# Optimization experiments

Hardware: AMD Instinct MI355X
Metric: run time of the kernel (lower is better)

The kernel has to match this reference:

```python
import jax, jax.numpy as jnp
import numpy as np
from jax import lax

M, T, D, E, NTAGS = 512, 512, 128, 512, 74
GH = D // 2   # GRU hidden per direction (64)
LH = E // 2   # LSTM hidden per direction (256)


def _gru_dir(x, Wih, Whh, bih, bhh):
    # x: [T, Din] -> [T, H]; PyTorch gate order r, z, n
    h = Whh.shape[1]
    gi = x @ Wih.T + bih  # [T, 3H] precomputed input projections
    def step(hprev, gi_t):
        gh = hprev @ Whh.T + bhh
        r = jax.nn.sigmoid(gi_t[:h] + gh[:h])
        z = jax.nn.sigmoid(gi_t[h:2 * h] + gh[h:2 * h])
        n = jnp.tanh(gi_t[2 * h:] + r * gh[2 * h:])
        hnew = (1.0 - z) * n + z * hprev
        return hnew, hnew
    _, hs = lax.scan(step, jnp.zeros((h,), x.dtype), gi)
    return hs


def _bigru(x, Wf, Uf, bf, cf, Wb, Ub, bb, cb):
    hf = _gru_dir(x, Wf, Uf, bf, cf)
    hb = _gru_dir(x[::-1], Wb, Ub, bb, cb)[::-1]
    return jnp.concatenate([hf, hb], axis=-1)


def _lstm_dir(x, Wih, Whh, bih, bhh):
    # PyTorch gate order i, f, g, o
    h = Whh.shape[1]
    gi = x @ Wih.T + bih  # [T, 4H]
    def step(carry, gi_t):
        hprev, cprev = carry
        g = gi_t + hprev @ Whh.T + bhh
        i = jax.nn.sigmoid(g[:h])
        f = jax.nn.sigmoid(g[h:2 * h])
        gg = jnp.tanh(g[2 * h:3 * h])
        o = jax.nn.sigmoid(g[3 * h:])
        c = f * cprev + i * gg
        hnew = o * jnp.tanh(c)
        return (hnew, c), hnew
    init = (jnp.zeros((h,), x.dtype), jnp.zeros((h,), x.dtype))
    _, hs = lax.scan(step, init, gi)
    return hs


def _bilstm(x, Wf, Uf, bf, cf, Wb, Ub, bb, cb):
    hf = _lstm_dir(x, Wf, Uf, bf, cf)
    hb = _lstm_dir(x[::-1], Wb, Ub, bb, cb)[::-1]
    return jnp.concatenate([hf, hb], axis=-1)


def setup_inputs() -> dict:
    key = jax.random.key(0)
    ks = jax.random.split(key, 32)
    s = 0.05
    def n(k, shape, scale=s):
        return jax.random.normal(k, shape, jnp.float32) * scale
    inp = {
        'memory': jax.random.normal(ks[0], (M, T, D), jnp.float32),
        'u': jax.random.normal(ks[1], (T, D), jnp.float32),
        'embed': jax.random.normal(ks[2], (T, E), jnp.float32),
        'W_ff': n(ks[3], (D, 2 * D)), 'b_ff': n(ks[4], (D,)),
        'gWih_f': n(ks[5], (3 * GH, D)), 'gWhh_f': n(ks[6], (3 * GH, GH)),
        'gbih_f': n(ks[7], (3 * GH,)), 'gbhh_f': n(ks[8], (3 * GH,)),
        'gWih_b': n(ks[9], (3 * GH, D)), 'gWhh_b': n(ks[10], (3 * GH, GH)),
        'gbih_b': n(ks[11], (3 * GH,)), 'gbhh_b': n(ks[12], (3 * GH,)),
        'W_k': n(ks[13], (E, D)), 'b_k': n(ks[14], (E,)),
        'lWih_f': n(ks[15], (4 * LH, E)), 'lWhh_f': n(ks[16], (4 * LH, LH)),
        'lbih_f': n(ks[17], (4 * LH,)), 'lbhh_f': n(ks[18], (4 * LH,)),
        'lWih_b': n(ks[19], (4 * LH, E)), 'lWhh_b': n(ks[20], (4 * LH, LH)),
        'lbih_b': n(ks[21], (4 * LH,)), 'lbhh_b': n(ks[22], (4 * LH,)),
        'W_out': n(ks[23], (NTAGS, E)), 'b_out': n(ks[24], (NTAGS,)),
    }
    return inp


def reference(memory, u, embed, W_ff, b_ff,
              gWih_f, gWhh_f, gbih_f, gbhh_f,
              gWih_b, gWhh_b, gbih_b, gbhh_b,
              W_k, b_k,
              lWih_f, lWhh_f, lbih_f, lbhh_f,
              lWih_b, lWhh_b, lbih_b, lbhh_b,
              W_out, b_out):
    # --- memory attention (original: python loop over self._memory) ---
    # p[i] = <flatten(memory[i]), flatten(u)>; softmax over memories
    p = jax.nn.softmax(jnp.einsum('mtd,td->m', memory, u))  # [M]
    cat = jnp.concatenate([memory, jnp.broadcast_to(u, memory.shape)], axis=-1)  # [M,T,2D]
    g = cat @ W_ff.T + b_ff  # [M,T,D] (ff_layer applied per memory)
    G = jnp.einsum('m,mtd->td', p, g)  # weighted sum over memories [T,D]
    # --- session encoder (bidirectional GRU) ---
    h = _bigru(G, gWih_f, gWhh_f, gbih_f, gbhh_f, gWib := gWih_b, gWhh_b, gbih_b, gbhh_b)  # [T,D]
    # --- knowledge encoder ---
    o = (u + h) @ W_k.T + b_k  # [T,E]
    # --- tagging head: BiLSTM over embed + o, then linear + softmax ---
    x = embed + o
    comb = _bilstm(x, lWih_f, lWhh_f, lbih_f, lbhh_f, lWih_b, lWhh_b, lbih_b, lbhh_b)  # [T,E]
    logits = comb @ W_out.T + b_out  # [T, NTAGS]
    return jax.nn.softmax(logits, axis=-1)
```

## Files before the change

kernel.cpp:

```cpp
#include <hip/hip_runtime.h>
#include <math.h>

#define TT 512
#define DD 128
#define MM 512
#define EE 512
#define NTAGS 74
#define GH 64
#define LH 256

typedef _Float16 half_t;
typedef _Float16 v2h __attribute__((ext_vector_type(2)));
typedef _Float16 v8h __attribute__((ext_vector_type(8)));
typedef _Float16 v16h __attribute__((ext_vector_type(16)));
typedef int v4i __attribute__((ext_vector_type(4)));

__device__ __forceinline__ float fdot2f(v2h a, v2h b, float c) {
#if __has_builtin(__builtin_amdgcn_fdot2)
    return __builtin_amdgcn_fdot2(a, b, c, false);
#else
    return c + (float)a[0] * (float)b[0] + (float)a[1] * (float)b[1];
#endif
}

__device__ __forceinline__ int sdot4(int a, int b, int c) {
#if __has_builtin(__builtin_amdgcn_sdot4)
    return __builtin_amdgcn_sdot4(a, b, c, false);
#else
    return c + ((a << 24) >> 24) * ((b << 24) >> 24)
             + ((a << 16) >> 24) * ((b << 16) >> 24)
             + ((a << 8) >> 24) * ((b << 8) >> 24)
             + (a >> 24) * (b >> 24);
#endif
}

__device__ __forceinline__ float sigf(float x) { return 1.f / (1.f + __expf(-x)); }
__device__ __forceinline__ float tanhfast(float x) { return 1.f - 2.f / (__expf(2.f * x) + 1.f); }

__device__ __forceinline__ void lds_barrier() {
    __builtin_amdgcn_sched_barrier(0);
    asm volatile("s_waitcnt lgkmcnt(0)" ::: "memory");
    __builtin_amdgcn_s_barrier();
    __builtin_amdgcn_sched_barrier(0);
}

__device__ __forceinline__ int qreduce_i(int x) {
    x += __builtin_amdgcn_mov_dpp(x, 0xB1, 0xF, 0xF, true);
    x += __builtin_amdgcn_mov_dpp(x, 0x4E, 0xF, 0xF, true);
    return x;
}
__device__ __forceinline__ float qreduce_f(float x) {
    x += __int_as_float(__builtin_amdgcn_mov_dpp(__float_as_int(x), 0xB1, 0xF, 0xF, true));
    x += __int_as_float(__builtin_amdgcn_mov_dpp(__float_as_int(x), 0x4E, 0xF, 0xF, true));
    return x;
}

__device__ __forceinline__ v16h load16(const float* p) {
    float4 x0 = ((const float4*)p)[0];
    float4 x1 = ((const float4*)p)[1];
    float4 x2 = ((const float4*)p)[2];
    float4 x3 = ((const float4*)p)[3];
    v16h r;
    r[0] = (half_t)x0.x; r[1] = (half_t)x0.y; r[2] = (half_t)x0.z; r[3] = (half_t)x0.w;
    r[4] = (half_t)x1.x; r[5] = (half_t)x1.y; r[6] = (half_t)x1.z; r[7] = (half_t)x1.w;
    r[8] = (half_t)x2.x; r[9] = (half_t)x2.y; r[10] = (half_t)x2.z; r[11] = (half_t)x2.w;
    r[12] = (half_t)x3.x; r[13] = (half_t)x3.y; r[14] = (half_t)x3.z; r[15] = (half_t)x3.w;
    return r;
}

#define OPAQUE3(a, b, c) asm volatile("" : "+v"(a), "+v"(b), "+v"(c))
#define OPAQUE4(a, b, c, d) asm volatile("" : "+v"(a), "+v"(b), "+v"(c), "+v"(d))

__device__ __forceinline__ void dot16(const v16h& w, const v8h& h0, const v8h& h1,
                                      float& x0, float& x1) {
    x0 = fdot2f(v2h{w[0], w[1]}, v2h{h0[0], h0[1]}, x0);
    x1 = fdot2f(v2h{w[2], w[3]}, v2h{h0[2], h0[3]}, x1);
    x0 = fdot2f(v2h{w[4], w[5]}, v2h{h0[4], h0[5]}, x0);
    x1 = fdot2f(v2h{w[6], w[7]}, v2h{h0[6], h0[7]}, x1);
    x0 = fdot2f(v2h{w[8], w[9]}, v2h{h1[0], h1[1]}, x0);
    x1 = fdot2f(v2h{w[10], w[11]}, v2h{h1[2], h1[3]}, x1);
    x0 = fdot2f(v2h{w[12], w[13]}, v2h{h1[4], h1[5]}, x0);
    x1 = fdot2f(v2h{w[14], w[15]}, v2h{h1[6], h1[7]}, x1);
}

__device__ __forceinline__ int pack4(int b0, int b1, int b2, int b3) {
    return (b0 & 0xff) | ((b1 & 0xff) << 8) | ((b2 & 0xff) << 16) | (b3 << 24);
}

__device__ __forceinline__ v4i quant16(const float* p, float inv_s) {
    float4 x0 = ((const float4*)p)[0];
    float4 x1 = ((const float4*)p)[1];
    float4 x2 = ((const float4*)p)[2];
    float4 x3 = ((const float4*)p)[3];
    v4i r;
    r.x = pack4(__float2int_rn(x0.x * inv_s), __float2int_rn(x0.y * inv_s),
                __float2int_rn(x0.z * inv_s), __float2int_rn(x0.w * inv_s));
    r.y = pack4(__float2int_rn(x1.x * inv_s), __float2int_rn(x1.y * inv_s),
                __float2int_rn(x1.z * inv_s), __float2int_rn(x1.w * inv_s));
    r.z = pack4(__float2int_rn(x2.x * inv_s), __float2int_rn(x2.y * inv_s),
                __float2int_rn(x2.z * inv_s), __float2int_rn(x2.w * inv_s));
    r.w = pack4(__float2int_rn(x3.x * inv_s), __float2int_rn(x3.y * inv_s),
                __float2int_rn(x3.z * inv_s), __float2int_rn(x3.w * inv_s));
    return r;
}

__device__ __forceinline__ float rowmax64(const float* p) {
    float m = 0.f;
#pragma unroll
    for (int k = 0; k < 64; k += 4) {
        float4 a = *(const float4*)(p + k);
        m = fmaxf(m, fmaxf(fmaxf(fabsf(a.x), fabsf(a.y)), fmaxf(fabsf(a.z), fabsf(a.w))));
    }
    return m;
}

__global__ __launch_bounds__(256) void k_dots(const float* __restrict__ mem,
                                              const float* __restrict__ u,
                                              float* __restrict__ dots) {
    int m = blockIdx.x;
    const float4* m4 = (const float4*)(mem + (size_t)m * TT * DD);
    const float4* u4 = (const float4*)u;
    float acc = 0.f;
#pragma unroll 4
    for (int it = 0; it < (TT * DD / 4) / 256; ++it) {
        int i = it * 256 + threadIdx.x;
        float4 a = m4[i], b = u4[i];
        acc += a.x * b.x + a.y * b.y + a.z * b.z + a.w * b.w;
    }
    for (int off = 32; off; off >>= 1) acc += __shfl_down(acc, off, 64);
    __shared__ float red[4];
    int w = threadIdx.x >> 6, l = threadIdx.x & 63;
    if (l == 0) red[w] = acc;
    __syncthreads();
    if (threadIdx.x == 0) dots[m] = red[0] + red[1] + red[2] + red[3];
}

__global__ __launch_bounds__(512) void k_softmax_p(const float* __restrict__ dots,
                                                   float* __restrict__ p) {
    int tid = threadIdx.x;
    float v = dots[tid];
    float mx = v;
    for (int off = 32; off; off >>= 1) mx = fmaxf(mx, __shfl_down(mx, off, 64));
    __shared__ float red[8];
    __shared__ float bm, bs;
    int w = tid >> 6, l = tid & 63;
    if (l == 0) red[w] = mx;
    __syncthreads();
    if (tid == 0) {
        float t = red[0];
        for (int i = 1; i < 8; ++i) t = fmaxf(t, red[i]);
        bm = t;
    }
    __syncthreads();
    float e = __expf(v - bm);
    float sm = e;
    for (int off = 32; off; off >>= 1) sm += __shfl_down(sm, off, 64);
    if (l == 0) red[w] = sm;
    __syncthreads();
    if (tid == 0) {
        float t = 0.f;
        for (int i = 0; i < 8; ++i) t += red[i];
        bs = t;
    }
    __syncthreads();
    p[tid] = e / bs;
}

__global__ __launch_bounds__(128) void k_wsum(const float* __restrict__ mem,
                                              const float* __restrict__ p,
                                              float* __restrict__ Mbar) {
    __shared__ float pl[MM];
    for (int i = threadIdx.x; i < MM; i += 128) pl[i] = p[i];
    __syncthreads();
    int i4 = blockIdx.x * 128 + threadIdx.x;
    const float4* m4 = (const float4*)mem;
    float4 acc = {0.f, 0.f, 0.f, 0.f};
#pragma unroll 4
    for (int m = 0; m < MM; ++m) {
        float pm = pl[m];
        float4 a = m4[(size_t)m * (TT * DD / 4) + i4];
        acc.x += pm * a.x; acc.y += pm * a.y; acc.z += pm * a.z; acc.w += pm * a.w;
    }
    ((float4*)Mbar)[i4] = acc;
}

__global__ __launch_bounds__(128) void k_G(const float* __restrict__ Mbar,
                                           const float* __restrict__ u,
                                           const float* __restrict__ Wff,
                                           const float* __restrict__ bff,
                                           float* __restrict__ G) {
    int t = blockIdx.x, d = threadIdx.x;
    __shared__ __align__(16) float Ml[DD], ul[DD];
    Ml[d] = Mbar[t * DD + d];
    ul[d] = u[t * DD + d];
    __syncthreads();
    const float* wr = Wff + (size_t)d * 2 * DD;
    float a0 = 0.f, a1 = 0.f;
#pragma unroll 4
    for (int k = 0; k < DD; ++k) {
        a0 += Ml[k] * wr[k];
        a1 += ul[k] * wr[DD + k];
    }
    G[t * DD + d] = a0 + a1 + bff[d];
}

__global__ __launch_bounds__(384) void k_gru_gi(const float* __restrict__ G,
                                                const float* __restrict__ Wf,
                                                const float* __restrict__ bf,
                                                const float* __restrict__ Wb,
                                                const float* __restrict__ bb,
                                                float* __restrict__ gi) {
    int t = blockIdx.x;
    __shared__ __align__(16) float Gl[DD];
    if (threadIdx.x < DD) Gl[threadIdx.x] = G[t * DD + threadIdx.x];
    __syncthreads();
    int r = threadIdx.x;
    const float* w;
    float b;
    float* o;
    if (r < 192) {
        w = Wf + (size_t)r * DD; b = bf[r]; o = gi + ((size_t)0 * TT + t) * 192 + r;
    } else {
        int rr = r - 192;
        w = Wb + (size_t)rr * DD; b = bb[rr]; o = gi + ((size_t)1 * TT + t) * 192 + rr;
    }
    float a0 = 0.f, a1 = 0.f;
#pragma unroll 4
    for (int k = 0; k < DD; k += 2) {
        a0 += Gl[k] * w[k];
        a1 += Gl[k + 1] * w[k + 1];
    }
    *o = a0 + a1 + b;
}

__global__ __launch_bounds__(256) void k_gru_seq(const float* __restrict__ Whh_f,
                                                 const float* __restrict__ bhh_f,
                                                 const float* __restrict__ Whh_b,
                                                 const float* __restrict__ bhh_b,
                                                 const float* __restrict__ gi,
                                                 float* __restrict__ hbufT) {
    int dir = blockIdx.x;
    int tid = threadIdx.x;
    int u = tid >> 2;
    int q = tid & 3;
    const float* Whh = dir ? Whh_b : Whh_f;
    const float* bhh = dir ? bhh_b : bhh_f;
    v16h wr = load16(Whh + (size_t)u * 64 + q * 16);
    v16h wz = load16(Whh + (size_t)(64 + u) * 64 + q * 16);
    v16h wn = load16(Whh + (size_t)(128 + u) * 64 + q * 16);
    OPAQUE3(wr, wz, wn);
    float bh_r = bhh[u], bh_z = bhh[64 + u], bh_n = bhh[128 + u];

    __shared__ __align__(16) half_t hl[2][64];
    if (tid < 64) hl[0][tid] = (half_t)0.f;
    float h = 0.f;
    int t0 = dir ? (TT - 1) : 0;
    const float* g0p = gi + ((size_t)dir * TT + t0) * 192 + u;
    float g_r = g0p[0], g_z = g0p[64], g_n = g0p[128];
    lds_barrier();

    float hs0 = 0.f, hs1 = 0.f, hs2 = 0.f, hs3 = 0.f;
#define GSTEP(J, HS) { \
    int s_ = s4 + (J); \
    int sn_ = (s_ + 1 < TT) ? (s_ + 1) : s_; \
    int tn_ = dir ? (TT - 1 - sn_) : sn_; \
    const float* gb_ = gi + ((size_t)dir * TT + tn_) * 192 + u; \
    float pr_ = gb_[0], pz_ = gb_[64], pn_ = gb_[128]; \
    const v8h* hv_ = (const v8h*)&hl[s_ & 1][q * 16]; \
    v8h h0_ = hv_[0], h1_ = hv_[1]; \
    float ar0 = 0.f, ar1 = 0.f, az0 = 0.f, az1 = 0.f, an0 = 0.f, an1 = 0.f; \
    dot16(wr, h0_, h1_, ar0, ar1); \
    dot16(wz, h0_, h1_, az0, az1); \
    dot16(wn, h0_, h1_, an0, an1); \
    float srd = qreduce_f(ar0 + ar1); \
    float szd = qreduce_f(az0 + az1); \
    float snd = qreduce_f(an0 + an1); \
    float r_ = sigf(g_r + srd + bh_r); \
    float z_ = sigf(g_z + szd + bh_z); \
    float n_ = tanhfast(g_n + r_ * (snd + bh_n)); \
    h = (1.f - z_) * n_ + z_ * h; \
    if (q == 0) hl[(s_ + 1) & 1][u] = (half_t)h; \
    HS = h; \
    lds_barrier(); \
    g_r = pr_; g_z = pz_; g_n = pn_; }

    for (int s4 = 0; s4 < TT; s4 += 4) {
        GSTEP(0, hs0);
        GSTEP(1, hs1);
        GSTEP(2, hs2);
        GSTEP(3, hs3);
        if (q == 0) {
            float4 v;
            int tb;
            if (dir == 0) { tb = s4; v = {hs0, hs1, hs2, hs3}; }
            else          { tb = TT - 4 - s4; v = {hs3, hs2, hs1, hs0}; }
            *(float4*)(hbufT + (size_t)(dir * 64 + u) * TT + tb) = v;
        }
    }
#undef GSTEP
}

__global__ __launch_bounds__(512) void k_x(const float* __restrict__ u,
                                           const float* __restrict__ hbufT,
                                           const float* __restrict__ Wk,
                                           const float* __restrict__ bk,
                                           const float* __restrict__ embed,
                                           float* __restrict__ x) {
    int t = blockIdx.x, e = threadIdx.x;
    __shared__ __align__(16) float sl[DD];
    if (e < DD) sl[e] = u[t * DD + e] + hbufT[(size_t)e * TT + t];
    __syncthreads();
    const float* wr = Wk + (size_t)e * DD;
    float a0 = 0.f, a1 = 0.f;
#pragma unroll 4
    for (int k = 0; k < DD; k += 2) {
        a0 += sl[k] * wr[k];
        a1 += sl[k + 1] * wr[k + 1];
    }
    x[t * EE + e] = embed[t * EE + e] + a0 + a1 + bk[e];
}

__global__ __launch_bounds__(1024) void k_lstm_gi(const float* __restrict__ x,
                                                  const float* __restrict__ Wf,
                                                  const float* __restrict__ bf,
                                                  const float* __restrict__ Wb,
                                                  const float* __restrict__ bb,
                                                  float* __restrict__ gi) {
    int dir = blockIdx.y;
    int t0 = blockIdx.x * 8;
    __shared__ __align__(16) float xl[8 * EE];
    for (int i = threadIdx.x; i < 8 * EE; i += 1024) xl[i] = x[(size_t)t0 * EE + i];
    __syncthreads();
    int r = threadIdx.x;
    const float* W = dir ? Wb : Wf;
    const float* bi = dir ? bb : bf;
    const float* wr = W + (size_t)r * EE;
    float b = bi[r];
    float acc[8];
#pragma unroll
    for (int uu = 0; uu < 8; ++uu) acc[uu] = b;
    for (int k = 0; k < EE; k += 4) {
        float4 wv = *(const float4*)(wr + k);
#pragma unroll
        for (int uu = 0; uu < 8; ++uu) {
            float4 xv = *(const float4*)(&xl[uu * EE + k]);
            acc[uu] += wv.x * xv.x + wv.y * xv.y + wv.z * xv.z + wv.w * xv.w;
        }
    }
#pragma unroll
    for (int uu = 0; uu < 8; ++uu)
        gi[((size_t)dir * TT + (t0 + uu)) * 1024 + r] = acc[uu];
}

__global__ __launch_bounds__(1024, 4) void k_lstm_seq(const float* __restrict__ Whh_f,
                                                      const float* __restrict__ bhh_f,
                                                      const float* __restrict__ Whh_b,
                                                      const float* __restrict__ bhh_b,
                                                      const float* __restrict__ gi,
                                                      float* __restrict__ combT) {
    int dir = blockIdx.x;
    int tid = threadIdx.x;
    int u = tid >> 2;
    int q = tid & 3;
    const float* Whh = dir ? Whh_b : Whh_f;
    const float* bhh = dir ? bhh_b : bhh_f;

    __shared__ __align__(16) int hq[2][64];

    const float* ri = Whh + (size_t)u * 256 + q * 64;
    const float* rf = ri + 256 * 256;
    const float* rg = ri + 512 * 256;
    const float* ro = ri + 768 * 256;

    float mi = rowmax64(ri); mi = fmaxf(mi, __shfl_xor(mi, 1, 64)); mi = fmaxf(mi, __shfl_xor(mi, 2, 64));
    float mf = rowmax64(rf); mf = fmaxf(mf, __shfl_xor(mf, 1, 64)); mf = fmaxf(mf, __shfl_xor(mf, 2, 64));
    float mg = rowmax64(rg); mg = fmaxf(mg, __shfl_xor(mg, 1, 64)); mg = fmaxf(mg, __shfl_xor(mg, 2, 64));
    float mo = rowmax64(ro); mo = fmaxf(mo, __shfl_xor(mo, 1, 64)); mo = fmaxf(mo, __shfl_xor(mo, 2, 64));
    float fs_i = mi / 16129.f, fs_f = mf / 16129.f, fs_g = mg / 16129.f, fs_o = mo / 16129.f;

    v4i wi0, wi1, wi2, wi3, wf0, wf1, wf2, wf3, wg0, wg1, wg2, wg3, wo0, wo1, wo2, wo3;
    {
        float inv_i = 127.f / mi, inv_f = 127.f / mf, inv_g = 127.f / mg, inv_o = 127.f / mo;
        wi0 = quant16(ri, inv_i); wi1 = quant16(ri + 16, inv_i);
        wi2 = quant16(ri + 32, inv_i); wi3 = quant16(ri + 48, inv_i);
        wf0 = quant16(rf, inv_f); wf1 = quant16(rf + 16, inv_f);
        wf2 = quant16(rf + 32, inv_f); wf3 = quant16(rf + 48, inv_f);
        wg0 = quant16(rg, inv_g); wg1 = quant16(rg + 16, inv_g);
        wg2 = quant16(rg + 32, inv_g); wg3 = quant16(rg + 48, inv_g);
        wo0 = quant16(ro, inv_o); wo1 = quant16(ro + 16, inv_o);
        wo2 = quant16(ro + 32, inv_o); wo3 = quant16(ro + 48, inv_o);
    }
    OPAQUE4(wi0, wi1, wi2, wi3);
    OPAQUE4(wf0, wf1, wf2, wf3);
    OPAQUE4(wg0, wg1, wg2, wg3);
    OPAQUE4(wo0, wo1, wo2, wo3);

    float bh_i = bhh[u], bh_f = bhh[256 + u], bh_g = bhh[512 + u], bh_o = bhh[768 + u];
    if (tid < 64) hq[0][tid] = 0;
    float c_state = 0.f;
    int tfirst = dir ? (TT - 1) : 0;
    const float* gp0 = gi + ((size_t)dir * TT + tfirst) * 1024 + u;
    float g_i = gp0[0], g_f = gp0[256], g_g = gp0[512], g_o = gp0[768];
    lds_barrier();

    float hs0 = 0.f, hs1 = 0.f, hs2 = 0.f, hs3 = 0.f;
#define LDOT(P, A0, A1) \
    A0 = sdot4((P##0).x, h0_.x, A0); A1 = sdot4((P##0).y, h0_.y, A1); \
    A0 = sdot4((P##0).z, h0_.z, A0); A1 = sdot4((P##0).w, h0_.w, A1); \
    A0 = sdot4((P##1).x, h1_.x, A0); A1 = sdot4((P##1).y, h1_.y, A1); \
    A0 = sdot4((P##1).z, h1_.z, A0); A1 = sdot4((P##1).w, h1_.w, A1); \
    A0 = sdot4((P##2).x, h2_.x, A0); A1 = sdot4((P##2).y, h2_.y, A1); \
    A0 = sdot4((P##2).z, h2_.z, A0); A1 = sdot4((P##2).w, h2_.w, A1); \
    A0 = sdot4((P##3).x, h3_.x, A0); A1 = sdot4((P##3).y, h3_.y, A1); \
    A0 = sdot4((P##3).z, h3_.z, A0); A1 = sdot4((P##3).w, h3_.w, A1)

#define LSTEP(J, HS) { \
    int s_ = s4 + (J); \
    int sn_ = (s_ + 1 < TT) ? (s_ + 1) : s_; \
    int tn_ = dir ? (TT - 1 - sn_) : sn_; \
    const float* gb_ = gi + ((size_t)dir * TT + tn_) * 1024 + u; \
    float pi_ = gb_[0], pf_ = gb_[256], pg_ = gb_[512], po_ = gb_[768]; \
    const v4i* hb_ = (const v4i*)&hq[s_ & 1][q * 16]; \
    v4i h0_ = hb_[0], h1_ = hb_[1], h2_ = hb_[2], h3_ = hb_[3]; \
    int ai0 = 0, ai1 = 0, af0 = 0, af1 = 0, ag0 = 0, ag1 = 0, ao0 = 0, ao1 = 0; \
    LDOT(wi, ai0, ai1); \
    LDOT(wf, af0, af1); \
    LDOT(wg, ag0, ag1); \
    LDOT(wo, ao0, ao1); \
    int ai_ = qreduce_i(ai0 + ai1); \
    int af_ = qreduce_i(af0 + af1); \
    int ag_ = qreduce_i(ag0 + ag1); \
    int ao_ = qreduce_i(ao0 + ao1); \
    float iv = sigf((float)ai_ * fs_i + bh_i + g_i); \
    float fv = sigf((float)af_ * fs_f + bh_f + g_f); \
    float gv = tanhfast((float)ag_ * fs_g + bh_g + g_g); \
    float ov = sigf((float)ao_ * fs_o + bh_o + g_o); \
    c_state = fv * c_state + iv * gv; \
    HS = ov * tanhfast(c_state); \
    if (q == 0) ((signed char*)hq[(s_ + 1) & 1])[u] = (signed char)__float2int_rn(HS * 127.f); \
    lds_barrier(); \
    g_i = pi_; g_f = pf_; g_g = pg_; g_o = po_; }

    for (int s4 = 0; s4 < TT; s4 += 4) {
        LSTEP(0, hs0);
        LSTEP(1, hs1);
        LSTEP(2, hs2);
        LSTEP(3, hs3);
        if (q == 0) {
            float4 v;
            int tb;
            if (dir == 0) { tb = s4; v = {hs0, hs1, hs2, hs3}; }
            else          { tb = TT - 4 - s4; v = {hs3, hs2, hs1, hs0}; }
            *(float4*)(combT + (size_t)(dir * 256 + u) * TT + tb) = v;
        }
    }
#undef LSTEP
#undef LDOT
}

__global__ __launch_bounds__(128) void k_out(const float* __restrict__ combT,
                                             const float* __restrict__ Wout,
                                             const float* __restrict__ bout,
                                             float* __restrict__ out) {
    int t = blockIdx.x;
    __shared__ __align__(16) float cl[EE];
    __shared__ float ll[NTAGS];
    __shared__ float mred, sred;
    for (int i = threadIdx.x; i < EE; i += 128) cl[i] = combT[(size_t)i * TT + t];
    __syncthreads();
    int e = threadIdx.x;
    if (e < NTAGS) {
        const float* wr = Wout + (size_t)e * EE;
        float a0 = 0.f, a1 = 0.f;
#pragma unroll 4
        for (int k = 0; k < EE; k += 2) {
            a0 += cl[k] * wr[k];
            a1 += cl[k + 1] * wr[k + 1];
        }
        ll[e] = a0 + a1 + bout[e];
    }
    __syncthreads();
    if (threadIdx.x == 0) {
        float m = ll[0];
        for (int i = 1; i < NTAGS; ++i) m = fmaxf(m, ll[i]);
        float ss = 0.f;
        for (int i = 0; i < NTAGS; ++i) ss += __expf(ll[i] - m);
        mred = m;
        sred = ss;
    }
    __syncthreads();
    if (e < NTAGS) out[t * NTAGS + e] = __expf(ll[e] - mred) / sred;
}

#define OFF_DOTS  ((size_t)0)
#define OFF_P     ((size_t)512)
#define OFF_MBAR  ((size_t)1024)
#define OFF_G     ((size_t)66560)
#define OFF_GIG   ((size_t)132096)
#define OFF_HBUF  ((size_t)328704)
#define OFF_X     ((size_t)394240)
#define OFF_GIL   ((size_t)656384)
#define OFF_COMB  ((size_t)1704960)

extern "C" void kernel_launch(void* const* d_in, const int* in_sizes, int n_in,
                              void* d_out, int out_size, void* d_ws, size_t ws_size,
                              hipStream_t stream) {
    const float* memory = (const float*)d_in[0];
    const float* u      = (const float*)d_in[1];
    const float* embed  = (const float*)d_in[2];
    const float* W_ff   = (const float*)d_in[3];
    const float* b_ff   = (const float*)d_in[4];
    const float* gWih_f = (const float*)d_in[5];
    const float* gWhh_f = (const float*)d_in[6];
    const float* gbih_f = (const float*)d_in[7];
    const float* gbhh_f = (const float*)d_in[8];
    const float* gWih_b = (const float*)d_in[9];
    const float* gWhh_b = (const float*)d_in[10];
    const float* gbih_b = (const float*)d_in[11];
    const float* gbhh_b = (const float*)d_in[12];
    const float* W_k    = (const float*)d_in[13];
    const float* b_k    = (const float*)d_in[14];
    const float* lWih_f = (const float*)d_in[15];
    const float* lWhh_f = (const float*)d_in[16];
    const float* lbih_f = (const float*)d_in[17];
    const float* lbhh_f = (const float*)d_in[18];
    const float* lWih_b = (const float*)d_in[19];
    const float* lWhh_b = (const float*)d_in[20];
    const float* lbih_b = (const float*)d_in[21];
    const float* lbhh_b = (const float*)d_in[22];
    const float* W_out  = (const float*)d_in[23];
    const float* b_out  = (const float*)d_in[24];
    float* out = (float*)d_out;
    float* ws = (float*)d_ws;

    float* dots  = ws + OFF_DOTS;
    float* p     = ws + OFF_P;
    float* Mbar  = ws + OFF_MBAR;
    float* G     = ws + OFF_G;
    float* giG   = ws + OFF_GIG;
    float* hbufT = ws + OFF_HBUF;
    float* x     = ws + OFF_X;
    float* giL   = ws + OFF_GIL;
    float* combT = ws + OFF_COMB;

    k_dots<<<MM, 256, 0, stream>>>(memory, u, dots);
    k_softmax_p<<<1, MM, 0, stream>>>(dots, p);
    k_wsum<<<128, 128, 0, stream>>>(memory, p, Mbar);
    k_G<<<TT, DD, 0, stream>>>(Mbar, u, W_ff, b_ff, G);
    k_gru_gi<<<TT, 384, 0, stream>>>(G, gWih_f, gbih_f, gWih_b, gbih_b, giG);
    k_gru_seq<<<2, 256, 0, stream>>>(gWhh_f, gbhh_f, gWhh_b, gbhh_b, giG, hbufT);
    k_x<<<TT, EE, 0, stream>>>(u, hbufT, W_k, b_k, embed, x);
    k_lstm_gi<<<dim3(64, 2), 1024, 0, stream>>>(x, lWih_f, lbih_f, lWih_b, lbih_b, giL);
    k_lstm_seq<<<2, 1024, 0, stream>>>(lWhh_f, lbhh_f, lWhh_b, lbhh_b, giL, combT);
    k_out<<<TT, 128, 0, stream>>>(combT, W_out, b_out, out);
}
```

Baseline: 1.398 ms.

## Halve LSTM recurrence threads per hidden unit and prefetch gate inputs four steps ahead

```diff
diff --git a/kernel.cpp b/kernel.cpp
--- a/kernel.cpp
+++ b/kernel.cpp
@@ -44,9 +44,8 @@
     __builtin_amdgcn_sched_barrier(0);
 }
 
-__device__ __forceinline__ int qreduce_i(int x) {
+__device__ __forceinline__ int preduce_i(int x) {
     x += __builtin_amdgcn_mov_dpp(x, 0xB1, 0xF, 0xF, true);
-    x += __builtin_amdgcn_mov_dpp(x, 0x4E, 0xF, 0xF, true);
     return x;
 }
 __device__ __forceinline__ float qreduce_f(float x) {
@@ -104,10 +103,10 @@
     return r;
 }
 
-__device__ __forceinline__ float rowmax64(const float* p) {
+__device__ __forceinline__ float rowmax128(const float* p) {
     float m = 0.f;
-#pragma unroll
-    for (int k = 0; k < 64; k += 4) {
+#pragma unroll 8
+    for (int k = 0; k < 128; k += 4) {
         float4 a = *(const float4*)(p + k);
         m = fmaxf(m, fmaxf(fmaxf(fabsf(a.x), fabsf(a.y)), fmaxf(fabsf(a.z), fabsf(a.w))));
     }
@@ -254,18 +253,18 @@
     __shared__ __align__(16) half_t hl[2][64];
     if (tid < 64) hl[0][tid] = (half_t)0.f;
     float h = 0.f;
-    int t0 = dir ? (TT - 1) : 0;
-    const float* g0p = gi + ((size_t)dir * TT + t0) * 192 + u;
-    float g_r = g0p[0], g_z = g0p[64], g_n = g0p[128];
+    float g0r, g0z, g0n, g1r, g1z, g1n, g2r, g2z, g2n, g3r, g3z, g3n;
+#define GPRO(J) { \
+    int tp_ = dir ? (TT - 1 - (J)) : (J); \
+    const float* gp_ = gi + ((size_t)dir * TT + tp_) * 192 + u; \
+    g##J##r = gp_[0]; g##J##z = gp_[64]; g##J##n = gp_[128]; }
+    GPRO(0); GPRO(1); GPRO(2); GPRO(3);
+#undef GPRO
     lds_barrier();
 
     float hs0 = 0.f, hs1 = 0.f, hs2 = 0.f, hs3 = 0.f;
 #define GSTEP(J, HS) { \
     int s_ = s4 + (J); \
-    int sn_ = (s_ + 1 < TT) ? (s_ + 1) : s_; \
-    int tn_ = dir ? (TT - 1 - sn_) : sn_; \
-    const float* gb_ = gi + ((size_t)dir * TT + tn_) * 192 + u; \
-    float pr_ = gb_[0], pz_ = gb_[64], pn_ = gb_[128]; \
     const v8h* hv_ = (const v8h*)&hl[s_ & 1][q * 16]; \
     v8h h0_ = hv_[0], h1_ = hv_[1]; \
     float ar0 = 0.f, ar1 = 0.f, az0 = 0.f, az1 = 0.f, an0 = 0.f, an1 = 0.f; \
@@ -275,14 +274,17 @@
     float srd = qreduce_f(ar0 + ar1); \
     float szd = qreduce_f(az0 + az1); \
     float snd = qreduce_f(an0 + an1); \
-    float r_ = sigf(g_r + srd + bh_r); \
-    float z_ = sigf(g_z + szd + bh_z); \
-    float n_ = tanhfast(g_n + r_ * (snd + bh_n)); \
+    float r_ = sigf(g##J##r + srd + bh_r); \
+    float z_ = sigf(g##J##z + szd + bh_z); \
+    float n_ = tanhfast(g##J##n + r_ * (snd + bh_n)); \
     h = (1.f - z_) * n_ + z_ * h; \
     if (q == 0) hl[(s_ + 1) & 1][u] = (half_t)h; \
     HS = h; \
-    lds_barrier(); \
-    g_r = pr_; g_z = pz_; g_n = pn_; }
+    int sp_ = s_ + 4; if (sp_ >= TT) sp_ = TT - 1; \
+    int tp_ = dir ? (TT - 1 - sp_) : sp_; \
+    const float* gp_ = gi + ((size_t)dir * TT + tp_) * 192 + u; \
+    g##J##r = gp_[0]; g##J##z = gp_[64]; g##J##n = gp_[128]; \
+    lds_barrier(); }
 
     for (int s4 = 0; s4 < TT; s4 += 4) {
         GSTEP(0, hs0);
@@ -352,101 +354,112 @@
         gi[((size_t)dir * TT + (t0 + uu)) * 1024 + r] = acc[uu];
 }
 
-__global__ __launch_bounds__(1024, 4) void k_lstm_seq(const float* __restrict__ Whh_f,
-                                                      const float* __restrict__ bhh_f,
-                                                      const float* __restrict__ Whh_b,
-                                                      const float* __restrict__ bhh_b,
-                                                      const float* __restrict__ gi,
-                                                      float* __restrict__ combT) {
+__global__ __launch_bounds__(512) __attribute__((amdgpu_waves_per_eu(2, 2)))
+void k_lstm_seq(const float* __restrict__ Whh_f,
+                const float* __restrict__ bhh_f,
+                const float* __restrict__ Whh_b,
+                const float* __restrict__ bhh_b,
+                const float* __restrict__ gi,
+                float* __restrict__ combT) {
     int dir = blockIdx.x;
     int tid = threadIdx.x;
-    int u = tid >> 2;
-    int q = tid & 3;
+    int u = tid >> 1;
+    int half = tid & 1;
     const float* Whh = dir ? Whh_b : Whh_f;
     const float* bhh = dir ? bhh_b : bhh_f;
 
     __shared__ __align__(16) int hq[2][64];
 
-    const float* ri = Whh + (size_t)u * 256 + q * 64;
+    const float* ri = Whh + (size_t)u * 256 + half * 128;
     const float* rf = ri + 256 * 256;
     const float* rg = ri + 512 * 256;
     const float* ro = ri + 768 * 256;
 
-    float mi = rowmax64(ri); mi = fmaxf(mi, __shfl_xor(mi, 1, 64)); mi = fmaxf(mi, __shfl_xor(mi, 2, 64));
-    float mf = rowmax64(rf); mf = fmaxf(mf, __shfl_xor(mf, 1, 64)); mf = fmaxf(mf, __shfl_xor(mf, 2, 64));
-    float mg = rowmax64(rg); mg = fmaxf(mg, __shfl_xor(mg, 1, 64)); mg = fmaxf(mg, __shfl_xor(mg, 2, 64));
-    float mo = rowmax64(ro); mo = fmaxf(mo, __shfl_xor(mo, 1, 64)); mo = fmaxf(mo, __shfl_xor(mo, 2, 64));
+    float mi = rowmax128(ri); mi = fmaxf(mi, __shfl_xor(mi, 1, 64));
+    float mf = rowmax128(rf); mf = fmaxf(mf, __shfl_xor(mf, 1, 64));
+    float mg = rowmax128(rg); mg = fmaxf(mg, __shfl_xor(mg, 1, 64));
+    float mo = rowmax128(ro); mo = fmaxf(mo, __shfl_xor(mo, 1, 64));
     float fs_i = mi / 16129.f, fs_f = mf / 16129.f, fs_g = mg / 16129.f, fs_o = mo / 16129.f;
 
-    v4i wi0, wi1, wi2, wi3, wf0, wf1, wf2, wf3, wg0, wg1, wg2, wg3, wo0, wo1, wo2, wo3;
+#define DECLG(P, ptr, inv)                                                        \
+    v4i P##0 = quant16((ptr), (inv)),       P##1 = quant16((ptr) + 16, (inv)),    \
+        P##2 = quant16((ptr) + 32, (inv)),  P##3 = quant16((ptr) + 48, (inv)),    \
+        P##4 = quant16((ptr) + 64, (inv)),  P##5 = quant16((ptr) + 80, (inv)),    \
+        P##6 = quant16((ptr) + 96, (inv)),  P##7 = quant16((ptr) + 112, (inv));   \
+    OPAQUE4(P##0, P##1, P##2, P##3);                                              \
+    OPAQUE4(P##4, P##5, P##6, P##7)
+
     {
-        float inv_i = 127.f / mi, inv_f = 127.f / mf, inv_g = 127.f / mg, inv_o = 127.f / mo;
-        wi0 = quant16(ri, inv_i); wi1 = quant16(ri + 16, inv_i);
-        wi2 = quant16(ri + 32, inv_i); wi3 = quant16(ri + 48, inv_i);
-        wf0 = quant16(rf, inv_f); wf1 = quant16(rf + 16, inv_f);
-        wf2 = quant16(rf + 32, inv_f); wf3 = quant16(rf + 48, inv_f);
-        wg0 = quant16(rg, inv_g); wg1 = quant16(rg + 16, inv_g);
-        wg2 = quant16(rg + 32, inv_g); wg3 = quant16(rg + 48, inv_g);
-        wo0 = quant16(ro, inv_o); wo1 = quant16(ro + 16, inv_o);
-        wo2 = quant16(ro + 32, inv_o); wo3 = quant16(ro + 48, inv_o);
-    }
-    OPAQUE4(wi0, wi1, wi2, wi3);
-    OPAQUE4(wf0, wf1, wf2, wf3);
-    OPAQUE4(wg0, wg1, wg2, wg3);
-    OPAQUE4(wo0, wo1, wo2, wo3);
+        float inv_i = 127.f / mi;
+        float inv_f = 127.f / mf;
+        float inv_g = 127.f / mg;
+        float inv_o = 127.f / mo;
+        (void)inv_i; (void)inv_f; (void)inv_g; (void)inv_o;
+    }
+    float inv_i = 127.f / mi, inv_f = 127.f / mf, inv_g = 127.f / mg, inv_o = 127.f / mo;
+    DECLG(wi, ri, inv_i);
+    DECLG(wf, rf, inv_f);
+    DECLG(wg, rg, inv_g);
+    DECLG(wo, ro, inv_o);
+#undef DECLG
 
     float bh_i = bhh[u], bh_f = bhh[256 + u], bh_g = bhh[512 + u], bh_o = bhh[768 + u];
     if (tid < 64) hq[0][tid] = 0;
     float c_state = 0.f;
-    int tfirst = dir ? (TT - 1) : 0;
-    const float* gp0 = gi + ((size_t)dir * TT + tfirst) * 1024 + u;
-    float g_i = gp0[0], g_f = gp0[256], g_g = gp0[512], g_o = gp0[768];
+
+    float g0i, g0f, g0g, g0o, g1i, g1f, g1g, g1o;
+    float g2i, g2f, g2g, g2o, g3i, g3f, g3g, g3o;
+#define LPRO(J) { \
+    int tp_ = dir ? (TT - 1 - (J)) : (J); \
+    const float* gp_ = gi + ((size_t)dir * TT + tp_) * 1024 + u; \
+    g##J##i = gp_[0]; g##J##f = gp_[256]; g##J##g = gp_[512]; g##J##o = gp_[768]; }
+    LPRO(0); LPRO(1); LPRO(2); LPRO(3);
+#undef LPRO
     lds_barrier();
 
     float hs0 = 0.f, hs1 = 0.f, hs2 = 0.f, hs3 = 0.f;
-#define LDOT(P, A0, A1) \
-    A0 = sdot4((P##0).x, h0_.x, A0); A1 = sdot4((P##0).y, h0_.y, A1); \
-    A0 = sdot4((P##0).z, h0_.z, A0); A1 = sdot4((P##0).w, h0_.w, A1); \
-    A0 = sdot4((P##1).x, h1_.x, A0); A1 = sdot4((P##1).y, h1_.y, A1); \
-    A0 = sdot4((P##1).z, h1_.z, A0); A1 = sdot4((P##1).w, h1_.w, A1); \
-    A0 = sdot4((P##2).x, h2_.x, A0); A1 = sdot4((P##2).y, h2_.y, A1); \
-    A0 = sdot4((P##2).z, h2_.z, A0); A1 = sdot4((P##2).w, h2_.w, A1); \
-    A0 = sdot4((P##3).x, h3_.x, A0); A1 = sdot4((P##3).y, h3_.y, A1); \
-    A0 = sdot4((P##3).z, h3_.z, A0); A1 = sdot4((P##3).w, h3_.w, A1)
+#define LD1(P, C, HV, A0, A1) \
+    A0 = sdot4((P##C).x, HV.x, A0); A1 = sdot4((P##C).y, HV.y, A1); \
+    A0 = sdot4((P##C).z, HV.z, A0); A1 = sdot4((P##C).w, HV.w, A1)
+#define LDOT8(P, A0, A1) \
+    LD1(P, 0, h0_, A0, A1); LD1(P, 1, h1_, A0, A1); \
+    LD1(P, 2, h2_, A0, A1); LD1(P, 3, h3_, A0, A1); \
+    LD1(P, 4, h4_, A0, A1); LD1(P, 5, h5_, A0, A1); \
+    LD1(P, 6, h6_, A0, A1); LD1(P, 7, h7_, A0, A1)
 
 #define LSTEP(J, HS) { \
     int s_ = s4 + (J); \
-    int sn_ = (s_ + 1 < TT) ? (s_ + 1) : s_; \
-    int tn_ = dir ? (TT - 1 - sn_) : sn_; \
-    const float* gb_ = gi + ((size_t)dir * TT + tn_) * 1024 + u; \
-    float pi_ = gb_[0], pf_ = gb_[256], pg_ = gb_[512], po_ = gb_[768]; \
-    const v4i* hb_ = (const v4i*)&hq[s_ & 1][q * 16]; \
+    const v4i* hb_ = (const v4i*)&hq[s_ & 1][half * 32]; \
     v4i h0_ = hb_[0], h1_ = hb_[1], h2_ = hb_[2], h3_ = hb_[3]; \
+    v4i h4_ = hb_[4], h5_ = hb_[5], h6_ = hb_[6], h7_ = hb_[7]; \
     int ai0 = 0, ai1 = 0, af0 = 0, af1 = 0, ag0 = 0, ag1 = 0, ao0 = 0, ao1 = 0; \
-    LDOT(wi, ai0, ai1); \
-    LDOT(wf, af0, af1); \
-    LDOT(wg, ag0, ag1); \
-    LDOT(wo, ao0, ao1); \
-    int ai_ = qreduce_i(ai0 + ai1); \
-    int af_ = qreduce_i(af0 + af1); \
-    int ag_ = qreduce_i(ag0 + ag1); \
-    int ao_ = qreduce_i(ao0 + ao1); \
-    float iv = sigf((float)ai_ * fs_i + bh_i + g_i); \
-    float fv = sigf((float)af_ * fs_f + bh_f + g_f); \
-    float gv = tanhfast((float)ag_ * fs_g + bh_g + g_g); \
-    float ov = sigf((float)ao_ * fs_o + bh_o + g_o); \
+    LDOT8(wi, ai0, ai1); \
+    LDOT8(wf, af0, af1); \
+    LDOT8(wg, ag0, ag1); \
+    LDOT8(wo, ao0, ao1); \
+    int ai_ = preduce_i(ai0 + ai1); \
+    int af_ = preduce_i(af0 + af1); \
+    int ag_ = preduce_i(ag0 + ag1); \
+    int ao_ = preduce_i(ao0 + ao1); \
+    float iv = sigf((float)ai_ * fs_i + bh_i + g##J##i); \
+    float fv = sigf((float)af_ * fs_f + bh_f + g##J##f); \
+    float gv = tanhfast((float)ag_ * fs_g + bh_g + g##J##g); \
+    float ov = sigf((float)ao_ * fs_o + bh_o + g##J##o); \
     c_state = fv * c_state + iv * gv; \
     HS = ov * tanhfast(c_state); \
-    if (q == 0) ((signed char*)hq[(s_ + 1) & 1])[u] = (signed char)__float2int_rn(HS * 127.f); \
-    lds_barrier(); \
-    g_i = pi_; g_f = pf_; g_g = pg_; g_o = po_; }
+    if (half == 0) ((signed char*)hq[(s_ + 1) & 1])[u] = (signed char)__float2int_rn(HS * 127.f); \
+    int sp_ = s_ + 4; if (sp_ >= TT) sp_ = TT - 1; \
+    int tp_ = dir ? (TT - 1 - sp_) : sp_; \
+    const float* gp_ = gi + ((size_t)dir * TT + tp_) * 1024 + u; \
+    g##J##i = gp_[0]; g##J##f = gp_[256]; g##J##g = gp_[512]; g##J##o = gp_[768]; \
+    lds_barrier(); }
 
     for (int s4 = 0; s4 < TT; s4 += 4) {
         LSTEP(0, hs0);
         LSTEP(1, hs1);
         LSTEP(2, hs2);
         LSTEP(3, hs3);
-        if (q == 0) {
+        if (half == 0) {
             float4 v;
             int tb;
             if (dir == 0) { tb = s4; v = {hs0, hs1, hs2, hs3}; }
@@ -455,7 +468,8 @@
         }
     }
 #undef LSTEP
-#undef LDOT
+#undef LDOT8
+#undef LD1
 }
 
 __global__ __launch_bounds__(128) void k_out(const float* __restrict__ combT,
@@ -551,6 +565,6 @@
     k_gru_seq<<<2, 256, 0, stream>>>(gWhh_f, gbhh_f, gWhh_b, gbhh_b, giG, hbufT);
     k_x<<<TT, EE, 0, stream>>>(u, hbufT, W_k, b_k, embed, x);
     k_lstm_gi<<<dim3(64, 2), 1024, 0, stream>>>(x, lWih_f, lbih_f, lWih_b, lbih_b, giL);
-    k_lstm_seq<<<2, 1024, 0, stream>>>(lWhh_f, lbhh_f, lWhh_b, lbhh_b, giL, combT);
+    k_lstm_seq<<<2, 512, 0, stream>>>(lWhh_f, lbhh_f, lWhh_b, lbhh_b, giL, combT);
     k_out<<<TT, 128, 0, stream>>>(combT, W_out, b_out, out);
 }
```

Measured after the change: 1.147 ms. -17.9%, faster.
